# Kernel tuning notes

Hardware: AMD Instinct MI355X
Metric: run time of the kernel (lower is better)

The kernel has to match this reference:

```python
import jax, jax.numpy as jnp
import numpy as np

N = 100000   # nodes
E = 400000   # edges
R = 237      # relations
D = 200      # feature dim (dims=[200,200,200])
B = 4096     # triple batch
L = 2        # num GAT layers
ALPHA = 0.01 # leaky-relu slope


def setup_inputs() -> dict:
    key = jax.random.key(0)
    ks = jax.random.split(key, 11)
    return dict(
        ent_embed=jax.random.normal(ks[0], (N, D), jnp.float32),
        rel_embed=jax.random.normal(ks[1], (R, D), jnp.float32),
        W_gat=jax.random.normal(ks[2], (L, D, D), jnp.float32) * 0.1,
        att_a=jax.random.normal(ks[3], (L, 2 * D), jnp.float32) * 0.1,
        W_hw=jax.random.normal(ks[4], (D, D), jnp.float32) * 0.1,
        b_hw=jax.random.normal(ks[5], (1, D), jnp.float32) * 0.1,
        edge_src=jax.random.randint(ks[6], (E,), 0, N),
        edge_dst=jax.random.randint(ks[7], (E,), 0, N),
        batch_h=jax.random.randint(ks[8], (B,), 0, N),
        batch_r=jax.random.randint(ks[9], (B,), 0, R),
        batch_t=jax.random.randint(ks[10], (B,), 0, N),
    )


def _gat_layer(x, W, a, src, dst):
    # x: [N,D], W: [D,D], a: [2D]
    Wh = x @ W                                  # [N,D]
    s_src = Wh @ a[:D]                          # [N] source score
    s_dst = Wh @ a[D:]                          # [N] dest score
    e = jax.nn.leaky_relu(s_src[src] + s_dst[dst], ALPHA)  # [E]
    # segment softmax over incoming edges of each destination node
    m = jax.ops.segment_max(e, dst, num_segments=N)
    m = jax.lax.stop_gradient(jnp.where(jnp.isfinite(m), m, 0.0))
    ex = jnp.exp(e - m[dst])
    denom = jax.ops.segment_sum(ex, dst, num_segments=N)
    att = ex / jnp.maximum(denom[dst], 1e-9)    # [E]
    out = jax.ops.segment_sum(att[:, None] * Wh[src], dst, num_segments=N)  # [N,D]
    return jax.nn.sigmoid(out)                  # act = torch.sigmoid, 1 head, concat=False


def reference(ent_embed, rel_embed, W_gat, att_a, W_hw, b_hw,
              edge_src, edge_dst, batch_h, batch_r, batch_t):
    x = ent_embed
    for i in range(L):
        gat_out = _gat_layer(x, W_gat[i], att_a[i], edge_src, edge_dst)
        # highway gate: sigma = sigmoid(x W + b); shared W,b across layers
        sigma = jax.nn.sigmoid(x @ W_hw + b_hw)
        x = sigma * gat_out + (1.0 - sigma) * x
    h = x[batch_h]
    r = rel_embed[batch_r]
    t = x[batch_t]
    return (h, r, t)
```

## Files before the change

### kernel.cpp

```cpp
#include <hip/hip_runtime.h>
#include <math.h>

#define NNODES 100000
#define NEDGES 400000
#define DIM    200
#define NB     4096
#define NL     2
#define ALPHA  0.01f
#define D4     (DIM/4)
#define NPAD   100096
#define KPAD   224
#define NKS    7
#define NCF    26
#define NBB    (2*NB)
#define NBLK   ((NNODES + 255) / 256)
#define SCAN_BPB 1024
#define NSB    ((NNODES + SCAN_BPB - 1) / SCAN_BPB)
#define GFULL  (NPAD / 32)
#define CSBLK  ((NPAD * 32) / 256)
#define PREPBLK ((2 * NKS * NCF * 64 + NL * 2 * DIM + 255) / 256)
#define SGB    (NBB / 32)
#define RELB   ((NB * D4 + 447) / 448)

typedef __attribute__((ext_vector_type(8))) short short8;
typedef __attribute__((ext_vector_type(4))) float f32x4;

__device__ __forceinline__ float sigm(float v) { return 1.0f / (1.0f + expf(-v)); }
__device__ __forceinline__ unsigned short f2bf(float f) {
    unsigned u = __float_as_uint(f);
    unsigned r = u + 0x7fff + ((u >> 16) & 1);
    return (unsigned short)(r >> 16);
}
__device__ __forceinline__ float bflo(unsigned u) { return __uint_as_float(u << 16); }
__device__ __forceinline__ float bfhi(unsigned u) { return __uint_as_float(u & 0xffff0000u); }

template<int MODE>
__global__ __launch_bounds__(256) void scanlb_k(const int* __restrict__ in,
                                                int* __restrict__ state,
                                                int* __restrict__ ticket,
                                                int* __restrict__ o0,
                                                int* __restrict__ o1,
                                                int* __restrict__ o2)
{
    __shared__ int sbid;
    __shared__ int tmp[256];
    __shared__ int sexcl;
    int tid = threadIdx.x;
    if (tid == 0) sbid = atomicAdd(ticket, 1);
    __syncthreads();
    int bid = sbid;
    int base = bid * SCAN_BPB + tid * 4;

    int4 v4 = make_int4(0, 0, 0, 0);
    if (base + 3 < NNODES) v4 = *(const int4*)(in + base);
    else {
        if (base + 0 < NNODES) v4.x = in[base + 0];
        if (base + 1 < NNODES) v4.y = in[base + 1];
        if (base + 2 < NNODES) v4.z = in[base + 2];
    }
    int s1 = v4.x + v4.y, s2 = s1 + v4.z, s3 = s2 + v4.w;

    tmp[tid] = s3; __syncthreads();
#pragma unroll
    for (int off = 1; off < 256; off <<= 1) {
        int t = (tid >= off) ? tmp[tid - off] : 0;
        __syncthreads();
        tmp[tid] += t;
        __syncthreads();
    }
    int bexcl_t = tmp[tid] - s3;
    int btotal  = tmp[255];

    if (tid == 0) {
        int st = (bid == 0) ? ((2 << 30) | btotal) : ((1 << 30) | btotal);
        __hip_atomic_store(&state[bid], st, __ATOMIC_RELEASE, __HIP_MEMORY_SCOPE_AGENT);
        if (bid == 0) sexcl = 0;
    }
    if (bid > 0 && tid < 64) {
        int excl = 0;
        int pred = bid - 1;
        while (pred >= -64) {
            int idx = pred - tid;
            int s = (idx >= 0)
                ? __hip_atomic_load(&state[idx], __ATOMIC_ACQUIRE, __HIP_MEMORY_SCOPE_AGENT)
                : (2 << 30);
            int f = ((unsigned)s) >> 30;
            unsigned long long nv = __ballot(f == 0);
            unsigned long long iv = __ballot(f == 2);
            int firstnv = nv ? (__ffsll(nv) - 1) : 64;
            int firstiv = iv ? (__ffsll(iv) - 1) : 64;
            if (firstiv < firstnv) {
                int contrib = (tid <= firstiv) ? (s & 0x3FFFFFFF) : 0;
#pragma unroll
                for (int m = 32; m; m >>= 1) contrib += __shfl_xor(contrib, m, 64);
                excl += contrib;
                break;
            } else if (firstnv > 0) {
                int contrib = (tid < firstnv) ? (s & 0x3FFFFFFF) : 0;
#pragma unroll
                for (int m = 32; m; m >>= 1) contrib += __shfl_xor(contrib, m, 64);
                excl += contrib;
                pred -= firstnv;
            }
        }
        if (tid == 0) {
            __hip_atomic_store(&state[bid], (2 << 30) | (excl + btotal),
                               __ATOMIC_RELEASE, __HIP_MEMORY_SCOPE_AGENT);
            sexcl = excl;
        }
    }
    __syncthreads();
    int ex = sexcl + bexcl_t;

    if (MODE == 0) {
        int4 r = make_int4(ex, ex + v4.x, ex + s1, ex + s2);
        if (base + 3 < NNODES) {
            *(int4*)(o0 + base) = r;
            *(int4*)(o1 + base) = r;
        } else {
            if (base + 0 < NNODES) { o0[base + 0] = r.x; o1[base + 0] = r.x; }
            if (base + 1 < NNODES) { o0[base + 1] = r.y; o1[base + 1] = r.y; }
            if (base + 2 < NNODES) { o0[base + 2] = r.z; o1[base + 2] = r.z; }
        }
        if (bid == NSB - 1 && tid == 0) o0[NNODES] = NEDGES;
    } else {
        int vv[4] = { v4.x, v4.y, v4.z, v4.w };
        int ee[4] = { ex, ex + v4.x, ex + s1, ex + s2 };
#pragma unroll
        for (int j = 0; j < 4; ++j) {
            int idx = base + j;
            if (idx < NNODES) {
                if (vv[j]) { o0[ee[j]] = idx; o1[idx] = ee[j]; }
                if (idx == NNODES - 1) *o2 = ee[j] + vv[j];
            }
        }
    }
}

__global__ void hist_k(const int* __restrict__ dst, int* __restrict__ deg)
{
    int e = blockIdx.x * blockDim.x + threadIdx.x;
    if (e < NEDGES) atomicAdd(&deg[dst[e]], 1);
}

__global__ void scatter_k(const int* __restrict__ src, const int* __restrict__ dst,
                          int* __restrict__ cursor, int* __restrict__ csr_src)
{
    int e = blockIdx.x * blockDim.x + threadIdx.x;
    if (e >= NEDGES) return;
    int d = dst[e];
    int p = atomicAdd(&cursor[d], 1);
    csr_src[p] = src[e];
}

__global__ void mark_k(const int* __restrict__ bh, const int* __restrict__ bt,
                       const int* __restrict__ rs, const int* __restrict__ csr_src,
                       int* __restrict__ mask)
{
    int e = blockIdx.x * 256 + threadIdx.x;
    if (e >= NBB) return;
    int node = (e < NB) ? bh[e] : bt[e - NB];
    mask[node] = 1;
    int b = rs[node], en = rs[node + 1];
    for (int j = b; j < en; ++j) mask[csr_src[j]] = 1;
}

__global__ __launch_bounds__(256) void zeroprep_k(int* __restrict__ deg, int* __restrict__ mask,
                                                  int* __restrict__ lbbuf,
                                                  const float* __restrict__ Wg,
                                                  const float* __restrict__ Whw,
                                                  const float* __restrict__ aa,
                                                  unsigned short* __restrict__ wp0,
                                                  unsigned short* __restrict__ wp1,
                                                  float* __restrict__ wv)
{
    int bid = blockIdx.x, tid = threadIdx.x;
    if (bid < NBLK) {
        int i = bid * 256 + tid;
        if (i < NNODES) { deg[i] = 0; mask[i] = 0; }
        if (i < 320) lbbuf[i] = 0;
        return;
    }
    int t0 = (bid - NBLK) * 256 + tid;
    const int WP = NKS * NCF * 64;
    if (t0 < 2 * WP) {
        int pk = (t0 >= WP) ? 1 : 0;
        int t = t0 - pk * WP;
        const float* Wgl = Wg + (size_t)pk * DIM * DIM;
        unsigned short* wp = pk ? wp1 : wp0;
        int l = t & 63, cf = (t >> 6) % NCF, ks = t / (NCF * 64);
        int col = (cf % 13) * 16 + (l & 15);
        const float* W = (cf < 13) ? Wgl : Whw;
        unsigned rr[4];
#pragma unroll
        for (int j = 0; j < 4; ++j) {
            int ka = ks * 32 + (l >> 4) * 8 + 2 * j;
            float fa = (ka < DIM && col < DIM) ? W[ka * DIM + col] : 0.f;
            float fb = (ka + 1 < DIM && col < DIM) ? W[(ka + 1) * DIM + col] : 0.f;
            rr[j] = (unsigned)f2bf(fa) | ((unsigned)f2bf(fb) << 16);
        }
        ((uint4*)wp)[t] = make_uint4(rr[0], rr[1], rr[2], rr[3]);
    } else {
        int u = t0 - 2 * WP;
        if (u >= NL * 2 * DIM) return;
        int l = u / (2 * DIM), sd = (u / DIM) % 2, k = u % DIM;
        const float* W = Wg + (size_t)l * DIM * DIM + (size_t)k * DIM;
        const float* av = aa + (size_t)l * 2 * DIM + sd * DIM;
        float s = 0.f;
        for (int c = 0; c < DIM; ++c) s = fmaf(W[c], av[c], s);
        wv[u] = s;
    }
}

__global__ __launch_bounds__(256) void convscore_k(const float* __restrict__ xin,
                                                   const float* __restrict__ wvl,
                                                   unsigned short* __restrict__ ap,
                                                   float* __restrict__ s_src,
                                                   float* __restrict__ s_dst)
{
    int gt = blockIdx.x * 256 + threadIdx.x;
    int row = gt >> 5, hl = gt & 31;
    if (row >= NPAD) return;

    float ps = 0.f, pd = 0.f;
    if (hl < 28) {
        uint4 o = make_uint4(0u, 0u, 0u, 0u);
        if (row < NNODES && hl < 25) {
            size_t base = (size_t)row * D4 + hl * 2;
            float4 x0 = ((const float4*)xin)[base];
            float4 x1 = ((const float4*)xin)[base + 1];
            o.x = (unsigned)f2bf(x0.x) | ((unsigned)f2bf(x0.y) << 16);
            o.y = (unsigned)f2bf(x0.z) | ((unsigned)f2bf(x0.w) << 16);
            o.z = (unsigned)f2bf(x1.x) | ((unsigned)f2bf(x1.y) << 16);
            o.w = (unsigned)f2bf(x1.z) | ((unsigned)f2bf(x1.w) << 16);
            float4 s0 = ((const float4*)wvl)[hl * 2];
            float4 s1 = ((const float4*)wvl)[hl * 2 + 1];
            float4 d0 = ((const float4*)(wvl + DIM))[hl * 2];
            float4 d1 = ((const float4*)(wvl + DIM))[hl * 2 + 1];
            ps = x0.x*s0.x + x0.y*s0.y + x0.z*s0.z + x0.w*s0.w
               + x1.x*s1.x + x1.y*s1.y + x1.z*s1.z + x1.w*s1.w;
            pd = x0.x*d0.x + x0.y*d0.y + x0.z*d0.z + x0.w*d0.w
               + x1.x*d1.x + x1.y*d1.y + x1.z*d1.z + x1.w*d1.w;
        }
        ((uint4*)ap)[(size_t)row * 28 + hl] = o;
    }
#pragma unroll
    for (int m = 16; m; m >>= 1) {
        ps += __shfl_xor(ps, m, 32);
        pd += __shfl_xor(pd, m, 32);
    }
    if (hl == 0 && row < NNODES) { s_src[row] = ps; s_dst[row] = pd; }
}

template<int CFBASE, int IND>
__device__ __forceinline__ void gemm_body(const unsigned short* __restrict__ Apack,
                                          const unsigned short* __restrict__ Wpack,
                                          const float* __restrict__ bhw,
                                          unsigned short* __restrict__ outb,
                                          const int* __restrict__ Lrow,
                                          const int* __restrict__ bh,
                                          const int* __restrict__ bt,
                                          int nrows, int vb, int tid)
{
    int rowbase = vb * 32;
    if (rowbase >= nrows) return;

    int w = tid >> 6;
    int l = tid & 63;
    int cgrp = l >> 4, cidx = l & 15;
    int cf0 = CFBASE + 2 * w;
    int cf1 = CFBASE + 2 * w + 1;
    int cf1l = (cf1 < NCF) ? cf1 : (NCF - 1);

    const short8* Bp = (const short8*)Wpack + l;
    short8 b0[NKS], b1[NKS];
#pragma unroll
    for (int ks = 0; ks < NKS; ++ks) {
        b0[ks] = Bp[(ks * NCF + cf0) * 64];
        b1[ks] = Bp[(ks * NCF + cf1l) * 64];
    }

    int e0 = rowbase + cidx, e1 = rowbase + 16 + cidx;
    int ar0, ar1;
    if (IND == 1) {
        ar0 = Lrow[min(e0, nrows - 1)];
        ar1 = Lrow[min(e1, nrows - 1)];
    } else if (IND == 2) {
        int c0 = min(e0, nrows - 1), c1 = min(e1, nrows - 1);
        ar0 = (c0 < NB) ? bh[c0] : bt[c0 - NB];
        ar1 = (c1 < NB) ? bh[c1] : bt[c1 - NB];
    } else { ar0 = e0; ar1 = e1; }

    const short8* Ap0 = (const short8*)(Apack + (size_t)ar0 * KPAD + cgrp * 8);
    const short8* Ap1 = (const short8*)(Apack + (size_t)ar1 * KPAD + cgrp * 8);

    f32x4 acc00 = (f32x4){0.f,0.f,0.f,0.f}, acc01 = acc00, acc10 = acc00, acc11 = acc00;

    short8 a0[2], a1[2];
    a0[0] = Ap0[0];
    a1[0] = Ap1[0];

#pragma unroll
    for (int ks = 0; ks < NKS; ++ks) {
        const int cur = ks & 1, nxt = cur ^ 1;
        if (ks + 1 < NKS) {
            a0[nxt] = Ap0[(ks + 1) * 4];
            a1[nxt] = Ap1[(ks + 1) * 4];
        }
        acc00 = __builtin_amdgcn_mfma_f32_16x16x32_bf16(a0[cur], b0[ks], acc00, 0, 0, 0);
        acc01 = __builtin_amdgcn_mfma_f32_16x16x32_bf16(a0[cur], b1[ks], acc01, 0, 0, 0);
        acc10 = __builtin_amdgcn_mfma_f32_16x16x32_bf16(a1[cur], b0[ks], acc10, 0, 0, 0);
        acc11 = __builtin_amdgcn_mfma_f32_16x16x32_bf16(a1[cur], b1[ks], acc11, 0, 0, 0);
    }

#pragma unroll
    for (int cc = 0; cc < 2; ++cc) {
        int cf = cc ? cf1 : cf0;
        if (cf >= CFBASE + 13) continue;
        int col = (cf - CFBASE) * 16 + cidx;
        if (col >= DIM) continue;
        f32x4 ar_0 = cc ? acc01 : acc00;
        f32x4 ar_1 = cc ? acc11 : acc10;
        if (CFBASE == 0) {
#pragma unroll
            for (int r = 0; r < 4; ++r) {
                int row = rowbase + cgrp * 4 + r;
                if (row < nrows) outb[(size_t)row * DIM + col] = f2bf(ar_0[r]);
                row += 16;
                if (row < nrows) outb[(size_t)row * DIM + col] = f2bf(ar_1[r]);
            }
        } else {
            float bb2 = bhw[col];
#pragma unroll
            for (int r = 0; r < 4; ++r) {
                int row = rowbase + cgrp * 4 + r;
                if (row < nrows) outb[(size_t)row * DIM + col] = f2bf(sigm(ar_0[r] + bb2));
                row += 16;
                if (row < nrows) outb[(size_t)row * DIM + col] = f2bf(sigm(ar_1[r] + bb2));
            }
        }
    }
}

__global__ __launch_bounds__(448) void gemm_whb_k(const unsigned short* __restrict__ Apack,
                                                  const unsigned short* __restrict__ Wpack,
                                                  unsigned short* __restrict__ whb)
{
    gemm_body<0, 0>(Apack, Wpack, nullptr, whb, nullptr, nullptr, nullptr,
                    NNODES, blockIdx.x, threadIdx.x);
}

__global__ __launch_bounds__(448) void gemm_sgc_k(const unsigned short* __restrict__ Apack,
                                                  const unsigned short* __restrict__ Wpack,
                                                  const float* __restrict__ bhw,
                                                  unsigned short* __restrict__ sgc,
                                                  const int* __restrict__ Lrow,
                                                  const int* __restrict__ nLp)
{
    gemm_body<13, 1>(Apack, Wpack, bhw, sgc, Lrow, nullptr, nullptr,
                     *nLp, blockIdx.x, threadIdx.x);
}

__global__ __launch_bounds__(256) void agg3c_k(const int* __restrict__ csr_src,
                                               const int* __restrict__ rs,
                                               const float* __restrict__ s_src,
                                               const float* __restrict__ s_dst,
                                               const unsigned short* __restrict__ whb,
                                               const unsigned short* __restrict__ sgc,
                                               unsigned short* __restrict__ apack,
                                               const int* __restrict__ Lrow,
                                               const int* __restrict__ nLp,
                                               const float* __restrict__ wvn,
                                               float* __restrict__ o_ssrc,
                                               float* __restrict__ o_sdst)
{
    int gt = blockIdx.x * 256 + threadIdx.x;
    int lidx = gt >> 5;
    int hl = gt & 31;
    if (lidx >= *nLp) return;
    int node = Lrow[lidx];

    int beg = rs[node], end = rs[node + 1];
    float sd = s_dst[node];

    float m = -3.4e38f;
    for (int j = beg + hl; j < end; j += 32) {
        float v = s_src[csr_src[j]] + sd;
        v = v > 0.f ? v : ALPHA * v;
        m = fmaxf(m, v);
    }
#pragma unroll
    for (int s = 16; s; s >>= 1) m = fmaxf(m, __shfl_xor(m, s, 32));
    float sum = 0.f;
    for (int j = beg + hl; j < end; j += 32) {
        float v = s_src[csr_src[j]] + sd;
        v = v > 0.f ? v : ALPHA * v;
        sum += expf(v - m);
    }
#pragma unroll
    for (int s = 16; s; s >>= 1) sum += __shfl_xor(sum, s, 32);
    float inv_ = 1.f / fmaxf(sum, 1e-9f);

    float ps = 0.f, pd = 0.f;
    if (hl < 25) {
        float av[8] = {0.f, 0.f, 0.f, 0.f, 0.f, 0.f, 0.f, 0.f};
        int j = beg;
        for (; j + 1 < end; j += 2) {
            int n0 = csr_src[j], n1 = csr_src[j + 1];
            float v0 = s_src[n0] + sd, v1 = s_src[n1] + sd;
            v0 = v0 > 0.f ? v0 : ALPHA * v0;
            v1 = v1 > 0.f ? v1 : ALPHA * v1;
            float c0 = expf(v0 - m) * inv_, c1 = expf(v1 - m) * inv_;
            uint4 w0 = ((const uint4*)whb)[(size_t)n0 * 25 + hl];
            uint4 w1 = ((const uint4*)whb)[(size_t)n1 * 25 + hl];
            av[0] = fmaf(c0, bflo(w0.x), av[0]); av[0] = fmaf(c1, bflo(w1.x), av[0]);
            av[1] = fmaf(c0, bfhi(w0.x), av[1]); av[1] = fmaf(c1, bfhi(w1.x), av[1]);
            av[2] = fmaf(c0, bflo(w0.y), av[2]); av[2] = fmaf(c1, bflo(w1.y), av[2]);
            av[3] = fmaf(c0, bfhi(w0.y), av[3]); av[3] = fmaf(c1, bfhi(w1.y), av[3]);
            av[4] = fmaf(c0, bflo(w0.z), av[4]); av[4] = fmaf(c1, bflo(w1.z), av[4]);
            av[5] = fmaf(c0, bfhi(w0.z), av[5]); av[5] = fmaf(c1, bfhi(w1.z), av[5]);
            av[6] = fmaf(c0, bflo(w0.w), av[6]); av[6] = fmaf(c1, bflo(w1.w), av[6]);
            av[7] = fmaf(c0, bfhi(w0.w), av[7]); av[7] = fmaf(c1, bfhi(w1.w), av[7]);
        }
        if (j < end) {
            int n0 = csr_src[j];
            float v0 = s_src[n0] + sd;
            v0 = v0 > 0.f ? v0 : ALPHA * v0;
            float c0 = expf(v0 - m) * inv_;
            uint4 w0 = ((const uint4*)whb)[(size_t)n0 * 25 + hl];
            av[0] = fmaf(c0, bflo(w0.x), av[0]);
            av[1] = fmaf(c0, bfhi(w0.x), av[1]);
            av[2] = fmaf(c0, bflo(w0.y), av[2]);
            av[3] = fmaf(c0, bfhi(w0.y), av[3]);
            av[4] = fmaf(c0, bflo(w0.z), av[4]);
            av[5] = fmaf(c0, bfhi(w0.z), av[5]);
            av[6] = fmaf(c0, bflo(w0.w), av[6]);
            av[7] = fmaf(c0, bfhi(w0.w), av[7]);
        }

        uint4 sv = ((const uint4*)sgc)[(size_t)lidx * 25 + hl];
        uint4 xv = ((const uint4*)apack)[(size_t)node * 28 + hl];
        float4 o0, o1;
        float s0;
        s0 = bflo(sv.x); o0.x = s0 * sigm(av[0]) + (1.f - s0) * bflo(xv.x);
        s0 = bfhi(sv.x); o0.y = s0 * sigm(av[1]) + (1.f - s0) * bfhi(xv.x);
        s0 = bflo(sv.y); o0.z = s0 * sigm(av[2]) + (1.f - s0) * bflo(xv.y);
        s0 = bfhi(sv.y); o0.w = s0 * sigm(av[3]) + (1.f - s0) * bfhi(xv.y);
        s0 = bflo(sv.z); o1.x = s0 * sigm(av[4]) + (1.f - s0) * bflo(xv.z);
        s0 = bfhi(sv.z); o1.y = s0 * sigm(av[5]) + (1.f - s0) * bfhi(xv.z);
        s0 = bflo(sv.w); o1.z = s0 * sigm(av[6]) + (1.f - s0) * bflo(xv.w);
        s0 = bfhi(sv.w); o1.w = s0 * sigm(av[7]) + (1.f - s0) * bfhi(xv.w);

        unsigned r0 = (unsigned)f2bf(o0.x) | ((unsigned)f2bf(o0.y) << 16);
        unsigned r1 = (unsigned)f2bf(o0.z) | ((unsigned)f2bf(o0.w) << 16);
        unsigned r2 = (unsigned)f2bf(o1.x) | ((unsigned)f2bf(o1.y) << 16);
        unsigned r3 = (unsigned)f2bf(o1.z) | ((unsigned)f2bf(o1.w) << 16);
        ((uint4*)apack)[(size_t)node * 28 + hl] = make_uint4(r0, r1, r2, r3);

        float4 ws0 = ((const float4*)wvn)[hl * 2];
        float4 ws1 = ((const float4*)wvn)[hl * 2 + 1];
        float4 wd0 = ((const float4*)(wvn + DIM))[hl * 2];
        float4 wd1 = ((const float4*)(wvn + DIM))[hl * 2 + 1];
        ps = o0.x*ws0.x + o0.y*ws0.y + o0.z*ws0.z + o0.w*ws0.w
           + o1.x*ws1.x + o1.y*ws1.y + o1.z*ws1.z + o1.w*ws1.w;
        pd = o0.x*wd0.x + o0.y*wd0.y + o0.z*wd0.z + o0.w*wd0.w
           + o1.x*wd1.x + o1.y*wd1.y + o1.z*wd1.z + o1.w*wd1.w;
    }
#pragma unroll
    for (int s = 16; s; s >>= 1) {
        ps += __shfl_xor(ps, s, 32);
        pd += __shfl_xor(pd, s, 32);
    }
    if (hl == 0) { o_ssrc[node] = ps; o_sdst[node] = pd; }
}

__global__ __launch_bounds__(448) void l1pack_k(const unsigned short* __restrict__ Apack,
                                                const unsigned short* __restrict__ Wpack1,
                                                const float* __restrict__ bhw,
                                                unsigned short* __restrict__ whc,
                                                unsigned short* __restrict__ sgbatch,
                                                const int* __restrict__ Lrow,
                                                const int* __restrict__ nLp,
                                                const int* __restrict__ bh,
                                                const int* __restrict__ bt,
                                                const float* __restrict__ rel,
                                                const int* __restrict__ br,
                                                float* __restrict__ out)
{
    int bid = blockIdx.x, tid = threadIdx.x;
    if (bid < GFULL) {
        gemm_body<0, 1>(Apack, Wpack1, bhw, whc, Lrow, nullptr, nullptr, *nLp, bid, tid);
    } else if (bid < GFULL + SGB) {
        gemm_body<13, 2>(Apack, Wpack1, bhw, sgbatch, nullptr, bh, bt, NBB, bid - GFULL, tid);
    } else {
        int u = (bid - GFULL - SGB) * 448 + tid;
        if (u < NB * D4) {
            int row = u / D4, c = u - row * D4;
            ((float4*)out)[(size_t)(NB + row) * D4 + c] =
                ((const float4*)rel)[(size_t)br[row] * D4 + c];
        }
    }
}

__global__ __launch_bounds__(256) void agg4_k(const int* __restrict__ csr_src,
                                              const int* __restrict__ rs,
                                              const float* __restrict__ s_src,
                                              const float* __restrict__ s_dst,
                                              const unsigned short* __restrict__ whc,
                                              const int* __restrict__ inv,
                                              const unsigned short* __restrict__ sgbatch,
                                              const unsigned short* __restrict__ apack,
                                              const int* __restrict__ bh,
                                              const int* __restrict__ bt,
                                              float* __restrict__ out)
{
    int gt = blockIdx.x * 256 + threadIdx.x;
    int e = gt >> 5;
    int hl = gt & 31;
    if (e >= NBB) return;
    int node = (e < NB) ? bh[e] : bt[e - NB];
    int orow = (e < NB) ? e : (2 * NB + (e - NB));

    int beg = rs[node], end = rs[node + 1];
    float sd = s_dst[node];

    float m = -3.4e38f;
    for (int j = beg + hl; j < end; j += 32) {
        float v = s_src[csr_src[j]] + sd;
        v = v > 0.f ? v : ALPHA * v;
        m = fmaxf(m, v);
    }
#pragma unroll
    for (int s = 16; s; s >>= 1) m = fmaxf(m, __shfl_xor(m, s, 32));
    float sum = 0.f;
    for (int j = beg + hl; j < end; j += 32) {
        float v = s_src[csr_src[j]] + sd;
        v = v > 0.f ? v : ALPHA * v;
        sum += expf(v - m);
    }
#pragma unroll
    for (int s = 16; s; s >>= 1) sum += __shfl_xor(sum, s, 32);
    float inv_ = 1.f / fmaxf(sum, 1e-9f);

    if (hl < 25) {
        float av[8] = {0.f, 0.f, 0.f, 0.f, 0.f, 0.f, 0.f, 0.f};
        int j = beg;
        for (; j + 1 < end; j += 2) {
            int n0 = csr_src[j], n1 = csr_src[j + 1];
            float v0 = s_src[n0] + sd, v1 = s_src[n1] + sd;
            v0 = v0 > 0.f ? v0 : ALPHA * v0;
            v1 = v1 > 0.f ? v1 : ALPHA * v1;
            float c0 = expf(v0 - m) * inv_, c1 = expf(v1 - m) * inv_;
            uint4 w0 = ((const uint4*)whc)[(size_t)inv[n0] * 25 + hl];
            uint4 w1 = ((const uint4*)whc)[(size_t)inv[n1] * 25 + hl];
            av[0] = fmaf(c0, bflo(w0.x), av[0]); av[0] = fmaf(c1, bflo(w1.x), av[0]);
            av[1] = fmaf(c0, bfhi(w0.x), av[1]); av[1] = fmaf(c1, bfhi(w1.x), av[1]);
            av[2] = fmaf(c0, bflo(w0.y), av[2]); av[2] = fmaf(c1, bflo(w1.y), av[2]);
            av[3] = fmaf(c0, bfhi(w0.y), av[3]); av[3] = fmaf(c1, bfhi(w1.y), av[3]);
            av[4] = fmaf(c0, bflo(w0.z), av[4]); av[4] = fmaf(c1, bflo(w1.z), av[4]);
            av[5] = fmaf(c0, bfhi(w0.z), av[5]); av[5] = fmaf(c1, bfhi(w1.z), av[5]);
            av[6] = fmaf(c0, bflo(w0.w), av[6]); av[6] = fmaf(c1, bflo(w1.w), av[6]);
            av[7] = fmaf(c0, bfhi(w0.w), av[7]); av[7] = fmaf(c1, bfhi(w1.w), av[7]);
        }
        if (j < end) {
            int n0 = csr_src[j];
            float v0 = s_src[n0] + sd;
            v0 = v0 > 0.f ? v0 : ALPHA * v0;
            float c0 = expf(v0 - m) * inv_;
            uint4 w0 = ((const uint4*)whc)[(size_t)inv[n0] * 25 + hl];
            av[0] = fmaf(c0, bflo(w0.x), av[0]);
            av[1] = fmaf(c0, bfhi(w0.x), av[1]);
            av[2] = fmaf(c0, bflo(w0.y), av[2]);
            av[3] = fmaf(c0, bfhi(w0.y), av[3]);
            av[4] = fmaf(c0, bflo(w0.z), av[4]);
            av[5] = fmaf(c0, bfhi(w0.z), av[5]);
            av[6] = fmaf(c0, bflo(w0.w), av[6]);
            av[7] = fmaf(c0, bfhi(w0.w), av[7]);
        }

        uint4 sv = ((const uint4*)sgbatch)[(size_t)e * 25 + hl];
        uint4 xv = ((const uint4*)apack)[(size_t)node * 28 + hl];
        float4 o0, o1;
        float s0;
        s0 = bflo(sv.x); o0.x = s0 * sigm(av[0]) + (1.f - s0) * bflo(xv.x);
        s0 = bfhi(sv.x); o0.y = s0 * sigm(av[1]) + (1.f - s0) * bfhi(xv.x);
        s0 = bflo(sv.y); o0.z = s0 * sigm(av[2]) + (1.f - s0) * bflo(xv.y);
        s0 = bfhi(sv.y); o0.w = s0 * sigm(av[3]) + (1.f - s0) * bfhi(xv.y);
        s0 = bflo(sv.z); o1.x = s0 * sigm(av[4]) + (1.f - s0) * bflo(xv.z);
        s0 = bfhi(sv.z); o1.y = s0 * sigm(av[5]) + (1.f - s0) * bfhi(xv.z);
        s0 = bflo(sv.w); o1.z = s0 * sigm(av[6]) + (1.f - s0) * bflo(xv.w);
        s0 = bfhi(sv.w); o1.w = s0 * sigm(av[7]) + (1.f - s0) * bfhi(xv.w);

        size_t base = (size_t)orow * D4 + hl * 2;
        ((float4*)out)[base]     = o0;
        ((float4*)out)[base + 1] = o1;
    }
}

extern "C" void kernel_launch(void* const* d_in, const int* in_sizes, int n_in,
                              void* d_out, int out_size, void* d_ws, size_t ws_size,
                              hipStream_t stream)
{
    const float* ent = (const float*)d_in[0];
    const float* rel = (const float*)d_in[1];
    const float* Wg  = (const float*)d_in[2];
    const float* aa  = (const float*)d_in[3];
    const float* Whw = (const float*)d_in[4];
    const float* bhw = (const float*)d_in[5];
    const int* esrc  = (const int*)d_in[6];
    const int* edst  = (const int*)d_in[7];
    const int* bh    = (const int*)d_in[8];
    const int* br    = (const int*)d_in[9];
    const int* bt    = (const int*)d_in[10];
    float* out = (float*)d_out;

    char* p = (char*)d_ws;
    auto carve = [&](size_t bytes) { char* r = p; p += (bytes + 63) & ~(size_t)63; return r; };
    unsigned short* whb     = (unsigned short*)carve((size_t)NNODES * DIM * 2);
    unsigned short* whc     = (unsigned short*)carve((size_t)NNODES * DIM * 2);
    unsigned short* sgc     = (unsigned short*)carve((size_t)NNODES * DIM * 2);
    unsigned short* apack   = (unsigned short*)carve((size_t)NPAD * KPAD * 2);
    unsigned short* sgbatch = (unsigned short*)carve((size_t)NBB * DIM * 2);
    unsigned short* wp0     = (unsigned short*)carve((size_t)NKS * NCF * 64 * 16);
    unsigned short* wp1     = (unsigned short*)carve((size_t)NKS * NCF * 64 * 16);
    float* wv    = (float*)carve(NL * 2 * DIM * 4);
    float* ss0   = (float*)carve(NNODES * 4);
    float* sd0   = (float*)carve(NNODES * 4);
    float* ss1   = (float*)carve(NNODES * 4);
    float* sd1   = (float*)carve(NNODES * 4);
    int* deg     = (int*)carve(NNODES * 4);
    int* rs      = (int*)carve((NNODES + 1) * 4);
    int* cursor  = (int*)carve(NNODES * 4);
    int* csr_src = (int*)carve(NEDGES * 4);
    int* mask    = (int*)carve(NNODES * 4);
    int* Lrow    = (int*)carve(NNODES * 4);
    int* inv     = (int*)carve(NNODES * 4);
    int* lbbuf   = (int*)carve(320 * 4);
    int* nLp     = (int*)carve(64);

    int* st0   = lbbuf;
    int* st1   = lbbuf + 128;
    int* tick0 = lbbuf + 256;
    int* tick1 = lbbuf + 257;

    zeroprep_k<<<NBLK + PREPBLK, 256, 0, stream>>>(deg, mask, lbbuf,
                                                   Wg, Whw, aa, wp0, wp1, wv);
    hist_k<<<(NEDGES + 255) / 256, 256, 0, stream>>>(edst, deg);
    scanlb_k<0><<<NSB, 256, 0, stream>>>(deg, st0, tick0, rs, cursor, nullptr);
    scatter_k<<<(NEDGES + 255) / 256, 256, 0, stream>>>(esrc, edst, cursor, csr_src);
    mark_k<<<(NBB + 255) / 256, 256, 0, stream>>>(bh, bt, rs, csr_src, mask);
    scanlb_k<1><<<NSB, 256, 0, stream>>>(mask, st1, tick1, Lrow, inv, nLp);

    convscore_k<<<(NPAD * 32) / 256, 256, 0, stream>>>(ent, wv, apack, ss0, sd0);

    gemm_whb_k<<<GFULL, 448, 0, stream>>>(apack, wp0, whb);
    gemm_sgc_k<<<GFULL, 448, 0, stream>>>(apack, wp0, bhw, sgc, Lrow, nLp);

    agg3c_k<<<(NNODES * 32) / 256, 256, 0, stream>>>(csr_src, rs, ss0, sd0, whb, sgc,
                                                     apack, Lrow, nLp, wv + 2 * DIM, ss1, sd1);

    l1pack_k<<<GFULL + SGB + RELB, 448, 0, stream>>>(apack, wp1, bhw, whc, sgbatch,
                                                     Lrow, nLp, bh, bt, rel, br, out);

    agg4_k<<<(NBB * 32) / 256, 256, 0, stream>>>(csr_src, rs, ss1, sd1, whc, inv,
                                                 sgbatch, apack, bh, bt, out);
}
```

Before: 212.1 us.

## Fuse bf16 conversion and attention scores into layer-0 GEMM, parallelize mark

Removes the separate convscore kernel that converted node features to packed bf16 and computed source/destination attention scores. The layer-0 GEMMs now read fp32 features directly, convert them to bf16 in registers, and produce the two score vectors from padding columns 200/201 of the packed weight, which now hold W·a. agg3c reads fp32 x instead of the packed bf16 copy. mark_k uses 32 lanes per batch node to walk neighbor lists. This saves one full pass over the feature matrix and a kernel launch. The cost is twice the fp32 A reads across the two GEMMs and attention scores computed from bf16 inputs.

```diff
diff --git a/kernel.cpp b/kernel.cpp
--- a/kernel.cpp
+++ b/kernel.cpp
@@ -17,7 +17,6 @@
 #define SCAN_BPB 1024
 #define NSB    ((NNODES + SCAN_BPB - 1) / SCAN_BPB)
 #define GFULL  (NPAD / 32)
-#define CSBLK  ((NPAD * 32) / 256)
 #define PREPBLK ((2 * NKS * NCF * 64 + NL * 2 * DIM + 255) / 256)
 #define SGB    (NBB / 32)
 #define RELB   ((NB * D4 + 447) / 448)
@@ -33,6 +32,20 @@
 }
 __device__ __forceinline__ float bflo(unsigned u) { return __uint_as_float(u << 16); }
 __device__ __forceinline__ float bfhi(unsigned u) { return __uint_as_float(u & 0xffff0000u); }
+
+__device__ __forceinline__ short8 ldAf(const float* __restrict__ p, int ka, int valid)
+{
+    short8 r = (short8){0,0,0,0,0,0,0,0};
+    if (valid && ka < DIM) {
+        float4 x0 = *(const float4*)(p);
+        float4 x1 = *(const float4*)(p + 4);
+        r[0] = (short)f2bf(x0.x); r[1] = (short)f2bf(x0.y);
+        r[2] = (short)f2bf(x0.z); r[3] = (short)f2bf(x0.w);
+        r[4] = (short)f2bf(x1.x); r[5] = (short)f2bf(x1.y);
+        r[6] = (short)f2bf(x1.z); r[7] = (short)f2bf(x1.w);
+    }
+    return r;
+}
 
 template<int MODE>
 __global__ __launch_bounds__(256) void scanlb_k(const int* __restrict__ in,
@@ -157,12 +170,13 @@
                        const int* __restrict__ rs, const int* __restrict__ csr_src,
                        int* __restrict__ mask)
 {
-    int e = blockIdx.x * 256 + threadIdx.x;
+    int g = blockIdx.x * 256 + threadIdx.x;
+    int e = g >> 5, hl = g & 31;
     if (e >= NBB) return;
     int node = (e < NB) ? bh[e] : bt[e - NB];
-    mask[node] = 1;
+    if (hl == 0) mask[node] = 1;
     int b = rs[node], en = rs[node + 1];
-    for (int j = b; j < en; ++j) mask[csr_src[j]] = 1;
+    for (int j = b + hl; j < en; j += 32) mask[csr_src[j]] = 1;
 }
 
 __global__ __launch_bounds__(256) void zeroprep_k(int* __restrict__ deg, int* __restrict__ mask,
@@ -195,8 +209,23 @@
 #pragma unroll
         for (int j = 0; j < 4; ++j) {
             int ka = ks * 32 + (l >> 4) * 8 + 2 * j;
-            float fa = (ka < DIM && col < DIM) ? W[ka * DIM + col] : 0.f;
-            float fb = (ka + 1 < DIM && col < DIM) ? W[(ka + 1) * DIM + col] : 0.f;
+            float fa = 0.f, fb = 0.f;
+            if (col < DIM) {
+                if (ka < DIM) fa = W[ka * DIM + col];
+                if (ka + 1 < DIM) fb = W[(ka + 1) * DIM + col];
+            } else if (pk == 0 && cf < 13 && col <= 201) {
+                const float* av = aa + (size_t)(col - 200) * DIM;
+                if (ka < DIM) {
+                    float s = 0.f;
+                    for (int c = 0; c < DIM; ++c) s = fmaf(Wgl[ka * DIM + c], av[c], s);
+                    fa = s;
+                }
+                if (ka + 1 < DIM) {
+                    float s = 0.f;
+                    for (int c = 0; c < DIM; ++c) s = fmaf(Wgl[(ka + 1) * DIM + c], av[c], s);
+                    fb = s;
+                }
+            }
             rr[j] = (unsigned)f2bf(fa) | ((unsigned)f2bf(fb) << 16);
         }
         ((uint4*)wp)[t] = make_uint4(rr[0], rr[1], rr[2], rr[3]);
@@ -212,54 +241,17 @@
     }
 }
 
-__global__ __launch_bounds__(256) void convscore_k(const float* __restrict__ xin,
-                                                   const float* __restrict__ wvl,
-                                                   unsigned short* __restrict__ ap,
-                                                   float* __restrict__ s_src,
-                                                   float* __restrict__ s_dst)
-{
-    int gt = blockIdx.x * 256 + threadIdx.x;
-    int row = gt >> 5, hl = gt & 31;
-    if (row >= NPAD) return;
-
-    float ps = 0.f, pd = 0.f;
-    if (hl < 28) {
-        uint4 o = make_uint4(0u, 0u, 0u, 0u);
-        if (row < NNODES && hl < 25) {
-            size_t base = (size_t)row * D4 + hl * 2;
-            float4 x0 = ((const float4*)xin)[base];
-            float4 x1 = ((const float4*)xin)[base + 1];
-            o.x = (unsigned)f2bf(x0.x) | ((unsigned)f2bf(x0.y) << 16);
-            o.y = (unsigned)f2bf(x0.z) | ((unsigned)f2bf(x0.w) << 16);
-            o.z = (unsigned)f2bf(x1.x) | ((unsigned)f2bf(x1.y) << 16);
-            o.w = (unsigned)f2bf(x1.z) | ((unsigned)f2bf(x1.w) << 16);
-            float4 s0 = ((const float4*)wvl)[hl * 2];
-            float4 s1 = ((const float4*)wvl)[hl * 2 + 1];
-            float4 d0 = ((const float4*)(wvl + DIM))[hl * 2];
-            float4 d1 = ((const float4*)(wvl + DIM))[hl * 2 + 1];
-            ps = x0.x*s0.x + x0.y*s0.y + x0.z*s0.z + x0.w*s0.w
-               + x1.x*s1.x + x1.y*s1.y + x1.z*s1.z + x1.w*s1.w;
-            pd = x0.x*d0.x + x0.y*d0.y + x0.z*d0.z + x0.w*d0.w
-               + x1.x*d1.x + x1.y*d1.y + x1.z*d1.z + x1.w*d1.w;
-        }
-        ((uint4*)ap)[(size_t)row * 28 + hl] = o;
-    }
-#pragma unroll
-    for (int m = 16; m; m >>= 1) {
-        ps += __shfl_xor(ps, m, 32);
-        pd += __shfl_xor(pd, m, 32);
-    }
-    if (hl == 0 && row < NNODES) { s_src[row] = ps; s_dst[row] = pd; }
-}
-
-template<int CFBASE, int IND>
+template<int CFBASE, int IND, int ASRC, int SC>
 __device__ __forceinline__ void gemm_body(const unsigned short* __restrict__ Apack,
+                                          const float* __restrict__ entp,
                                           const unsigned short* __restrict__ Wpack,
                                           const float* __restrict__ bhw,
                                           unsigned short* __restrict__ outb,
                                           const int* __restrict__ Lrow,
                                           const int* __restrict__ bh,
                                           const int* __restrict__ bt,
+                                          float* __restrict__ ssc,
+                                          float* __restrict__ sdc,
                                           int nrows, int vb, int tid)
 {
     int rowbase = vb * 32;
@@ -281,7 +273,7 @@
     }
 
     int e0 = rowbase + cidx, e1 = rowbase + 16 + cidx;
-    int ar0, ar1;
+    int ar0, ar1, v0 = 1, v1 = 1;
     if (IND == 1) {
         ar0 = Lrow[min(e0, nrows - 1)];
         ar1 = Lrow[min(e1, nrows - 1)];
@@ -289,23 +281,38 @@
         int c0 = min(e0, nrows - 1), c1 = min(e1, nrows - 1);
         ar0 = (c0 < NB) ? bh[c0] : bt[c0 - NB];
         ar1 = (c1 < NB) ? bh[c1] : bt[c1 - NB];
-    } else { ar0 = e0; ar1 = e1; }
-
-    const short8* Ap0 = (const short8*)(Apack + (size_t)ar0 * KPAD + cgrp * 8);
-    const short8* Ap1 = (const short8*)(Apack + (size_t)ar1 * KPAD + cgrp * 8);
+    } else {
+        v0 = e0 < nrows; v1 = e1 < nrows;
+        ar0 = min(e0, nrows - 1); ar1 = min(e1, nrows - 1);
+    }
+
+    const short8* Ap0; const short8* Ap1;
+    const float* Fp0; const float* Fp1;
+    if (ASRC == 0) {
+        Ap0 = (const short8*)(Apack + (size_t)ar0 * KPAD + cgrp * 8);
+        Ap1 = (const short8*)(Apack + (size_t)ar1 * KPAD + cgrp * 8);
+    } else {
+        Fp0 = entp + (size_t)ar0 * DIM + cgrp * 8;
+        Fp1 = entp + (size_t)ar1 * DIM + cgrp * 8;
+    }
 
     f32x4 acc00 = (f32x4){0.f,0.f,0.f,0.f}, acc01 = acc00, acc10 = acc00, acc11 = acc00;
 
     short8 a0[2], a1[2];
-    a0[0] = Ap0[0];
-    a1[0] = Ap1[0];
+    if (ASRC == 0) { a0[0] = Ap0[0]; a1[0] = Ap1[0]; }
+    else { a0[0] = ldAf(Fp0, cgrp * 8, v0); a1[0] = ldAf(Fp1, cgrp * 8, v1); }
 
 #pragma unroll
     for (int ks = 0; ks < NKS; ++ks) {
         const int cur = ks & 1, nxt = cur ^ 1;
         if (ks + 1 < NKS) {
-            a0[nxt] = Ap0[(ks + 1) * 4];
-            a1[nxt] = Ap1[(ks + 1) * 4];
+            if (ASRC == 0) {
+                a0[nxt] = Ap0[(ks + 1) * 4];
+                a1[nxt] = Ap1[(ks + 1) * 4];
+            } else {
+                a0[nxt] = ldAf(Fp0 + (ks + 1) * 32, cgrp * 8 + (ks + 1) * 32, v0);
+                a1[nxt] = ldAf(Fp1 + (ks + 1) * 32, cgrp * 8 + (ks + 1) * 32, v1);
+            }
         }
         acc00 = __builtin_amdgcn_mfma_f32_16x16x32_bf16(a0[cur], b0[ks], acc00, 0, 0, 0);
         acc01 = __builtin_amdgcn_mfma_f32_16x16x32_bf16(a0[cur], b1[ks], acc01, 0, 0, 0);
@@ -318,9 +325,21 @@
         int cf = cc ? cf1 : cf0;
         if (cf >= CFBASE + 13) continue;
         int col = (cf - CFBASE) * 16 + cidx;
-        if (col >= DIM) continue;
         f32x4 ar_0 = cc ? acc01 : acc00;
         f32x4 ar_1 = cc ? acc11 : acc10;
+        if (col >= DIM) {
+            if (SC && CFBASE == 0 && col <= 201) {
+                float* so = (col == 200) ? ssc : sdc;
+#pragma unroll
+                for (int r = 0; r < 4; ++r) {
+                    int row = rowbase + cgrp * 4 + r;
+                    if (row < nrows) so[row] = ar_0[r];
+                    row += 16;
+                    if (row < nrows) so[row] = ar_1[r];
+                }
+            }
+            continue;
+        }
         if (CFBASE == 0) {
 #pragma unroll
             for (int r = 0; r < 4; ++r) {
@@ -342,23 +361,25 @@
     }
 }
 
-__global__ __launch_bounds__(448) void gemm_whb_k(const unsigned short* __restrict__ Apack,
-                                                  const unsigned short* __restrict__ Wpack,
-                                                  unsigned short* __restrict__ whb)
-{
-    gemm_body<0, 0>(Apack, Wpack, nullptr, whb, nullptr, nullptr, nullptr,
-                    NNODES, blockIdx.x, threadIdx.x);
-}
-
-__global__ __launch_bounds__(448) void gemm_sgc_k(const unsigned short* __restrict__ Apack,
+__global__ __launch_bounds__(448) void gemm_whbsc_k(const float* __restrict__ ent,
+                                                    const unsigned short* __restrict__ Wpack,
+                                                    unsigned short* __restrict__ whb,
+                                                    float* __restrict__ ss0,
+                                                    float* __restrict__ sd0)
+{
+    gemm_body<0, 0, 1, 1>(nullptr, ent, Wpack, nullptr, whb, nullptr, nullptr, nullptr,
+                          ss0, sd0, NNODES, blockIdx.x, threadIdx.x);
+}
+
+__global__ __launch_bounds__(448) void gemm_sgc_k(const float* __restrict__ ent,
                                                   const unsigned short* __restrict__ Wpack,
                                                   const float* __restrict__ bhw,
                                                   unsigned short* __restrict__ sgc,
                                                   const int* __restrict__ Lrow,
                                                   const int* __restrict__ nLp)
 {
-    gemm_body<13, 1>(Apack, Wpack, bhw, sgc, Lrow, nullptr, nullptr,
-                     *nLp, blockIdx.x, threadIdx.x);
+    gemm_body<13, 1, 1, 0>(nullptr, ent, Wpack, bhw, sgc, Lrow, nullptr, nullptr,
+                           nullptr, nullptr, *nLp, blockIdx.x, threadIdx.x);
 }
 
 __global__ __launch_bounds__(256) void agg3c_k(const int* __restrict__ csr_src,
@@ -367,6 +388,7 @@
                                                const float* __restrict__ s_dst,
                                                const unsigned short* __restrict__ whb,
                                                const unsigned short* __restrict__ sgc,
+                                               const float* __restrict__ xin,
                                                unsigned short* __restrict__ apack,
                                                const int* __restrict__ Lrow,
                                                const int* __restrict__ nLp,
@@ -439,17 +461,18 @@
         }
 
         uint4 sv = ((const uint4*)sgc)[(size_t)lidx * 25 + hl];
-        uint4 xv = ((const uint4*)apack)[(size_t)node * 28 + hl];
+        float4 xa = ((const float4*)xin)[(size_t)node * D4 + hl * 2];
+        float4 xb = ((const float4*)xin)[(size_t)node * D4 + hl * 2 + 1];
         float4 o0, o1;
         float s0;
-        s0 = bflo(sv.x); o0.x = s0 * sigm(av[0]) + (1.f - s0) * bflo(xv.x);
-        s0 = bfhi(sv.x); o0.y = s0 * sigm(av[1]) + (1.f - s0) * bfhi(xv.x);
-        s0 = bflo(sv.y); o0.z = s0 * sigm(av[2]) + (1.f - s0) * bflo(xv.y);
-        s0 = bfhi(sv.y); o0.w = s0 * sigm(av[3]) + (1.f - s0) * bfhi(xv.y);
-        s0 = bflo(sv.z); o1.x = s0 * sigm(av[4]) + (1.f - s0) * bflo(xv.z);
-        s0 = bfhi(sv.z); o1.y = s0 * sigm(av[5]) + (1.f - s0) * bfhi(xv.z);
-        s0 = bflo(sv.w); o1.z = s0 * sigm(av[6]) + (1.f - s0) * bflo(xv.w);
-        s0 = bfhi(sv.w); o1.w = s0 * sigm(av[7]) + (1.f - s0) * bfhi(xv.w);
+        s0 = bflo(sv.x); o0.x = s0 * sigm(av[0]) + (1.f - s0) * xa.x;
+        s0 = bfhi(sv.x); o0.y = s0 * sigm(av[1]) + (1.f - s0) * xa.y;
+        s0 = bflo(sv.y); o0.z = s0 * sigm(av[2]) + (1.f - s0) * xa.z;
+        s0 = bfhi(sv.y); o0.w = s0 * sigm(av[3]) + (1.f - s0) * xa.w;
+        s0 = bflo(sv.z); o1.x = s0 * sigm(av[4]) + (1.f - s0) * xb.x;
+        s0 = bfhi(sv.z); o1.y = s0 * sigm(av[5]) + (1.f - s0) * xb.y;
+        s0 = bflo(sv.w); o1.z = s0 * sigm(av[6]) + (1.f - s0) * xb.z;
+        s0 = bfhi(sv.w); o1.w = s0 * sigm(av[7]) + (1.f - s0) * xb.w;
 
         unsigned r0 = (unsigned)f2bf(o0.x) | ((unsigned)f2bf(o0.y) << 16);
         unsigned r1 = (unsigned)f2bf(o0.z) | ((unsigned)f2bf(o0.w) << 16);
@@ -489,9 +512,11 @@
 {
     int bid = blockIdx.x, tid = threadIdx.x;
     if (bid < GFULL) {
-        gemm_body<0, 1>(Apack, Wpack1, bhw, whc, Lrow, nullptr, nullptr, *nLp, bid, tid);
+        gemm_body<0, 1, 0, 0>(Apack, nullptr, Wpack1, bhw, whc, Lrow, nullptr, nullptr,
+                              nullptr, nullptr, *nLp, bid, tid);
     } else if (bid < GFULL + SGB) {
-        gemm_body<13, 2>(Apack, Wpack1, bhw, sgbatch, nullptr, bh, bt, NBB, bid - GFULL, tid);
+        gemm_body<13, 2, 0, 0>(Apack, nullptr, Wpack1, bhw, sgbatch, nullptr, bh, bt,
+                               nullptr, nullptr, NBB, bid - GFULL, tid);
     } else {
         int u = (bid - GFULL - SGB) * 448 + tid;
         if (u < NB * D4) {
@@ -648,16 +673,15 @@
     hist_k<<<(NEDGES + 255) / 256, 256, 0, stream>>>(edst, deg);
     scanlb_k<0><<<NSB, 256, 0, stream>>>(deg, st0, tick0, rs, cursor, nullptr);
     scatter_k<<<(NEDGES + 255) / 256, 256, 0, stream>>>(esrc, edst, cursor, csr_src);
-    mark_k<<<(NBB + 255) / 256, 256, 0, stream>>>(bh, bt, rs, csr_src, mask);
+    mark_k<<<(NBB * 32 + 255) / 256, 256, 0, stream>>>(bh, bt, rs, csr_src, mask);
     scanlb_k<1><<<NSB, 256, 0, stream>>>(mask, st1, tick1, Lrow, inv, nLp);
 
-    convscore_k<<<(NPAD * 32) / 256, 256, 0, stream>>>(ent, wv, apack, ss0, sd0);
-
-    gemm_whb_k<<<GFULL, 448, 0, stream>>>(apack, wp0, whb);
-    gemm_sgc_k<<<GFULL, 448, 0, stream>>>(apack, wp0, bhw, sgc, Lrow, nLp);
+    gemm_whbsc_k<<<GFULL, 448, 0, stream>>>(ent, wp0, whb, ss0, sd0);
+    gemm_sgc_k<<<GFULL, 448, 0, stream>>>(ent, wp0, bhw, sgc, Lrow, nLp);
 
     agg3c_k<<<(NNODES * 32) / 256, 256, 0, stream>>>(csr_src, rs, ss0, sd0, whb, sgc,
-                                                     apack, Lrow, nLp, wv + 2 * DIM, ss1, sd1);
+                                                     ent, apack, Lrow, nLp,
+                                                     wv + 2 * DIM, ss1, sd1);
 
     l1pack_k<<<GFULL + SGB + RELB, 448, 0, stream>>>(apack, wp1, bhw, whc, sgbatch,
                                                      Lrow, nLp, bh, bt, rel, br, out);
```

After: 245.6 us. 1.16x slower.
